# Kernel optimization log

Hardware: AMD Instinct MI355X
Metric: run time of the kernel (lower is better)

Reference implementation:

```python
import jax, jax.numpy as jnp
import numpy as np

ROPE_BASE = 10000.0

def _rope_tables(seq_len, head_dim, dtype):
    inv_freq = 1.0 / (ROPE_BASE ** (jnp.arange(0, head_dim, 2, dtype=jnp.float32) / head_dim))
    t = jnp.arange(seq_len, dtype=jnp.float32)
    freqs = jnp.einsum('s,d->sd', t, inv_freq)  # [S, D/2]
    return jnp.cos(freqs).astype(dtype), jnp.sin(freqs).astype(dtype)

def _apply_rope(x, cos, sin):
    # x: [B, H, S, D]; cos/sin: [S, D/2]
    half = x.shape[-1] // 2
    x1, x2 = x[..., :half], x[..., half:]
    c = cos[None, None, :, :]
    s = sin[None, None, :, :]
    return jnp.concatenate([x1 * c - x2 * s, x1 * s + x2 * c], axis=-1)

def setup_inputs() -> dict:
    key = jax.random.key(0)
    k1, k2, k3 = jax.random.split(key, 3)
    B, S, dim = 4, 2048, 1024
    x = jax.random.normal(k1, (B, S, dim), dtype=jnp.float32)
    Wqkv = jax.random.normal(k2, (3 * dim, dim), dtype=jnp.float32) * (1.0 / np.sqrt(dim))
    Wout = jax.random.normal(k3, (dim, dim), dtype=jnp.float32) * (1.0 / np.sqrt(dim))
    mask = jnp.tril(jnp.ones((S, S), dtype=bool))[None, None, :, :]  # causal [1,1,S,S]
    return {"x": x, "mask": mask, "Wqkv": Wqkv, "Wout": Wout, "n_heads": 16}

def reference(x, mask, Wqkv, Wout, n_heads):
    B, S, dim = x.shape
    H = n_heads
    D = dim // H
    qkv = jnp.einsum('bsd,ed->bse', x, Wqkv)             # [B,S,3*dim]
    qkv = qkv.reshape(B, S, 3, H, D)
    q = jnp.transpose(qkv[:, :, 0], (0, 2, 1, 3))        # [B,H,S,D]
    k = jnp.transpose(qkv[:, :, 1], (0, 2, 1, 3))
    v = jnp.transpose(qkv[:, :, 2], (0, 2, 1, 3))
    cos, sin = _rope_tables(S, D, x.dtype)
    q = _apply_rope(q, cos, sin)
    k = _apply_rope(k, cos, sin)
    scale = 1.0 / np.sqrt(D).astype(np.float32)
    scores = jnp.einsum('bhsd,bhtd->bhst', q, k) * scale  # [B,H,S,S]
    scores = jnp.where(mask, scores, -jnp.inf)
    attn = jax.nn.softmax(scores, axis=-1)
    out = jnp.einsum('bhst,bhtd->bhsd', attn, v)          # [B,H,S,D]
    out = jnp.transpose(out, (0, 2, 1, 3)).reshape(B, S, dim)
    return jnp.einsum('bsd,ed->bse', out, Wout)
```

## Files before the change

kernel.cpp:

```cpp
#include <hip/hip_runtime.h>
#include <math.h>


typedef __attribute__((ext_vector_type(8))) __bf16 bf16x8;
typedef __attribute__((ext_vector_type(8))) short  short8;
typedef __attribute__((ext_vector_type(4))) short  s16x4;
typedef __attribute__((ext_vector_type(4))) float  f32x4;

#define MFMA16(a, b, c) __builtin_amdgcn_mfma_f32_16x16x32_bf16((a), (b), (c), 0, 0, 0)

static constexpr int    BATCH = 4;
static constexpr int    SEQ   = 2048;
static constexpr int    DIM   = 1024;
static constexpr int    NH    = 16;
static constexpr int    HD    = 64;
static constexpr size_t BHSD  = (size_t)BATCH * NH * SEQ * HD;
static constexpr float  NEGINF = -1e9f;
static constexpr int    PS_LD  = 72;

__device__ __forceinline__ short f2bf(float f) {
    union { float f; unsigned u; } v; v.f = f;
    unsigned r = v.u + 0x7fffu + ((v.u >> 16) & 1u);
    return (short)(r >> 16);
}

__device__ __forceinline__ short8 cvt8(const f32x4 lo, const f32x4 hi) {
    short8 r;
    r[0] = f2bf(lo[0]); r[1] = f2bf(lo[1]); r[2] = f2bf(lo[2]); r[3] = f2bf(lo[3]);
    r[4] = f2bf(hi[0]); r[5] = f2bf(hi[1]); r[6] = f2bf(hi[2]); r[7] = f2bf(hi[3]);
    return r;
}

template <bool F32>
__device__ __forceinline__ short8 ld8(const void* p, size_t row, int K, int k) {
    if constexpr (F32) {
        const float* f = (const float*)p;
        f32x4 lo = *(const f32x4*)&f[row * (size_t)K + k];
        f32x4 hi = *(const f32x4*)&f[row * (size_t)K + k + 4];
        return cvt8(lo, hi);
    } else {
        const short* s = (const short*)p;
        return *(const short8*)&s[row * (size_t)K + k];
    }
}

__device__ __forceinline__ void gload16(const void* g, void* lds) {
    __builtin_amdgcn_global_load_lds(
        (const __attribute__((address_space(1))) void*)g,
        (__attribute__((address_space(3))) void*)lds, 16, 0, 0);
}

__global__ __launch_bounds__(256) void prep_kernel(
    const float* __restrict__ X, const float* __restrict__ Wq,
    const float* __restrict__ Wo, short* __restrict__ Xb,
    short* __restrict__ Wqb, short* __restrict__ Wob,
    float* __restrict__ cosT, float* __restrict__ sinT) {
    const int stride = gridDim.x * blockDim.x;
    for (int idx = blockIdx.x * blockDim.x + threadIdx.x; idx < 3211264; idx += stride) {
        if (idx < 3145728) {
            const float* src; short* dst; int off;
            if (idx < 2097152)      { src = X;  dst = Xb;  off = idx; }
            else if (idx < 2883584) { src = Wq; dst = Wqb; off = idx - 2097152; }
            else                    { src = Wo; dst = Wob; off = idx - 2883584; }
            f32x4 v = *(const f32x4*)&src[(size_t)off * 4];
            s16x4 r;
            r[0] = f2bf(v[0]); r[1] = f2bf(v[1]); r[2] = f2bf(v[2]); r[3] = f2bf(v[3]);
            *(s16x4*)&dst[(size_t)off * 4] = r;
        } else {
            int r = idx - 3145728;
            int s = r >> 5, d = r & 31;
            float ang = (float)s * __expf(-0.28782313662425574f * (float)d);
            float sn, cs;
            sincosf(ang, &sn, &cs);
            cosT[r] = cs; sinT[r] = sn;
        }
    }
}

template <bool AF32, bool BF32>
__device__ __forceinline__ void gemm128_core(
    const void* __restrict__ A, const void* __restrict__ B, int K,
    short* As, short* Bs, int bm, int bn, f32x4 acc[4][4]) {
    const int tid  = threadIdx.x;
    const int lane = tid & 63;
    const int wave = tid >> 6;
    const int quad = lane >> 4;
    const int col  = lane & 15;
    const int wm   = (wave & 1) * 64;
    const int wn   = (wave >> 1) * 64;

    const int r0 = tid >> 2;
    const int r1 = (tid + 256) >> 2;
    const int ko = (tid & 3) * 8;

#pragma unroll
    for (int i = 0; i < 4; ++i)
#pragma unroll
        for (int j = 0; j < 4; ++j) acc[i][j] = f32x4{0.f, 0.f, 0.f, 0.f};

#pragma unroll 1
    for (int k0 = 0; k0 < K; k0 += 32) {
        short8 a0 = ld8<AF32>(A, (size_t)(bm + r0), K, k0 + ko);
        short8 a1 = ld8<AF32>(A, (size_t)(bm + r1), K, k0 + ko);
        short8 b0 = ld8<BF32>(B, (size_t)(bn + r0), K, k0 + ko);
        short8 b1 = ld8<BF32>(B, (size_t)(bn + r1), K, k0 + ko);
        __syncthreads();
        *(short8*)&As[tid * 8]         = a0;
        *(short8*)&As[(tid + 256) * 8] = a1;
        *(short8*)&Bs[tid * 8]         = b0;
        *(short8*)&Bs[(tid + 256) * 8] = b1;
        __syncthreads();

        bf16x8 af[4], bfr[4];
#pragma unroll
        for (int i = 0; i < 4; ++i)
            af[i] = *(const bf16x8*)&As[(wm + i * 16 + col) * 32 + quad * 8];
#pragma unroll
        for (int j = 0; j < 4; ++j)
            bfr[j] = *(const bf16x8*)&Bs[(wn + j * 16 + col) * 32 + quad * 8];
#pragma unroll
        for (int i = 0; i < 4; ++i)
#pragma unroll
            for (int j = 0; j < 4; ++j)
                acc[i][j] = MFMA16(af[i], bfr[j], acc[i][j]);
    }
}

__device__ __forceinline__ void gemm128_p2(
    const short* __restrict__ A, const short* __restrict__ B, int K,
    short* As, short* Bs, int bm, int bn, f32x4 acc[4][4]) {
    const int tid  = threadIdx.x;
    const int lane = tid & 63;
    const int wave = tid >> 6;
    const int quad = lane >> 4;
    const int col  = lane & 15;
    const int wm   = (wave & 1) * 64;
    const int wn   = (wave >> 1) * 64;

    const int nt = K >> 6;
    const int rr = tid >> 3;
    const int swk = (((tid & 7) ^ (rr & 7)) << 3);
    const short* Ab = &A[(size_t)(bm + rr) * K + swk];
    const short* Bb = &B[(size_t)(bn + rr) * K + swk];

#pragma unroll
    for (int i = 0; i < 4; ++i)
#pragma unroll
        for (int j = 0; j < 4; ++j) acc[i][j] = f32x4{0.f, 0.f, 0.f, 0.f};

#define STAGE_TILE(c)                                                         \
    {                                                                         \
        const int s_ = (c) & 1;                                               \
        const int k0_ = (c) << 6;                                             \
        _Pragma("unroll")                                                     \
        for (int q = 0; q < 4; ++q) {                                         \
            gload16(Ab + (size_t)(q * 32) * K + k0_,                          \
                    &As[s_ * 8192 + q * 2048 + wave * 512]);                  \
            gload16(Bb + (size_t)(q * 32) * K + k0_,                          \
                    &Bs[s_ * 8192 + q * 2048 + wave * 512]);                  \
        }                                                                     \
    }

    STAGE_TILE(0);
    STAGE_TILE(1);

    const int pc0 = ((quad) ^ (col & 7)) << 3;
    const int pc1 = ((4 | quad) ^ (col & 7)) << 3;

#pragma unroll 1
    for (int c = 0; c < nt; ++c) {
        const int s = c & 1;
        if (c + 1 < nt) { asm volatile("s_waitcnt vmcnt(8)" ::: "memory"); }
        else            { asm volatile("s_waitcnt vmcnt(0)" ::: "memory"); }
        __builtin_amdgcn_s_barrier();

        const short* Asl = &As[s * 8192];
        const short* Bsl = &Bs[s * 8192];
        bf16x8 af[4][2], bfr[4][2];
#pragma unroll
        for (int i = 0; i < 4; ++i) {
            const int r = (wm + i * 16 + col) * 64;
            af[i][0] = *(const bf16x8*)&Asl[r + pc0];
            af[i][1] = *(const bf16x8*)&Asl[r + pc1];
        }
#pragma unroll
        for (int j = 0; j < 4; ++j) {
            const int r = (wn + j * 16 + col) * 64;
            bfr[j][0] = *(const bf16x8*)&Bsl[r + pc0];
            bfr[j][1] = *(const bf16x8*)&Bsl[r + pc1];
        }
#pragma unroll
        for (int kk = 0; kk < 2; ++kk)
#pragma unroll
            for (int i = 0; i < 4; ++i)
#pragma unroll
                for (int j = 0; j < 4; ++j)
                    acc[i][j] = MFMA16(af[i][kk], bfr[j][kk], acc[i][j]);

        __builtin_amdgcn_s_barrier();
        if (c + 2 < nt) STAGE_TILE(c + 2);
    }
#undef STAGE_TILE
}

template <bool PRE>
__global__ __launch_bounds__(256, 2) void qkv_rope_kernel(
    const void* __restrict__ X, const void* __restrict__ W,
    const float* __restrict__ cosT, const float* __restrict__ sinT,
    short* __restrict__ Qo, short* __restrict__ Ko, short* __restrict__ VT) {
    __shared__ __align__(16) short As[2 * 8192];
    __shared__ __align__(16) short Bs[2 * 8192];
    const int bm = blockIdx.y * 128, bn = blockIdx.x * 128;
    const int lane = threadIdx.x & 63, wave = threadIdx.x >> 6;
    const int quad = lane >> 4, col = lane & 15;
    const int wm = (wave & 1) * 64, wn = (wave >> 1) * 64;

    f32x4 acc[4][4];
    if constexpr (PRE)
        gemm128_p2((const short*)X, (const short*)W, 1024, As, Bs, bm, bn, acc);
    else
        gemm128_core<true, true>(X, W, 1024, As, Bs, bm, bn, acc);

    const int n0    = bn + wn;
    const int which = n0 >> 10;
    const int h     = (n0 >> 6) & 15;

    if (which == 2) {
#pragma unroll
        for (int i = 0; i < 4; ++i) {
            int    m = bm + wm + i * 16 + quad * 4;
            int    b = m >> 11, s = m & 2047;
            size_t rowb = (size_t)(b * NH + h) * HD;
#pragma unroll
            for (int j = 0; j < 4; ++j) {
                int   d = j * 16 + col;
                s16x4 pk;
                pk[0] = f2bf(acc[i][j][0]); pk[1] = f2bf(acc[i][j][1]);
                pk[2] = f2bf(acc[i][j][2]); pk[3] = f2bf(acc[i][j][3]);
                *(s16x4*)&VT[(rowb + d) * SEQ + s] = pk;
            }
        }
    } else {
        short* dst = which ? Ko : Qo;
#pragma unroll
        for (int i = 0; i < 4; ++i)
#pragma unroll
            for (int reg = 0; reg < 4; ++reg) {
                int    m = bm + wm + i * 16 + quad * 4 + reg;
                int    b = m >> 11, s = m & 2047;
                size_t base = ((size_t)(b * NH + h) * SEQ + s) * HD;
#pragma unroll
                for (int j = 0; j < 2; ++j) {
                    int   d1 = j * 16 + col;
                    float sn, cs;
                    if constexpr (PRE) {
                        cs = cosT[(s << 5) + d1];
                        sn = sinT[(s << 5) + d1];
                    } else {
                        float inv = __expf(-0.28782313662425574f * (float)d1);
                        sincosf((float)s * inv, &sn, &cs);
                    }
                    float x1 = acc[i][j][reg];
                    float x2 = acc[i][j + 2][reg];
                    dst[base + d1]      = f2bf(x1 * cs - x2 * sn);
                    dst[base + d1 + 32] = f2bf(x1 * sn + x2 * cs);
                }
            }
    }
}

__global__ __launch_bounds__(256, 2) void attn_kernel(
    const short* __restrict__ Q, const short* __restrict__ K,
    const short* __restrict__ VT, short* __restrict__ att) {
    const int b = blockIdx.z, h = blockIdx.y;
    const int tid = threadIdx.x, wave = tid >> 6, lane = tid & 63;
    const int quad = lane >> 4, col = lane & 15;
    const size_t hoff = (size_t)(b * NH + h) * SEQ * HD;
    const short* Qp  = Q + hoff;
    const short* Kp  = K + hoff;
    const short* VTp = VT + hoff;

    __shared__ __align__(16) short Kt[64 * 64];
    __shared__ __align__(16) short Vt[64 * 64];
    __shared__ __align__(16) short Ps[4 * 32 * PS_LD];

    const int r0 = tid >> 3;
    const int r1 = r0 + 32;
    const int c8 = (tid & 7) * 8;
    const int cs = c8 ^ ((r0 & 7) << 3);
    const int swc = (col & 7) << 3;
    const int cA  = (quad * 8) ^ swc;
    const int cB  = (32 + quad * 8) ^ swc;
    short* Pw = &Ps[wave * 32 * PS_LD];

#pragma unroll 1
    for (int pass = 0; pass < 2; ++pass) {
        const int qt   = pass ? 15 - (int)blockIdx.x : (int)blockIdx.x;
        const int q0   = qt * 128 + wave * 32;
        const int tmax = 2 * qt + 1;

        bf16x8 aq[2][2];
#pragma unroll
        for (int s2 = 0; s2 < 2; ++s2) {
            aq[s2][0] = *(const bf16x8*)&Qp[(q0 + s2 * 16 + col) * HD + quad * 8];
            aq[s2][1] = *(const bf16x8*)&Qp[(q0 + s2 * 16 + col) * HD + 32 + quad * 8];
        }

        float m_i[2][4], l_i[2][4];
        f32x4 o[2][4];
#pragma unroll
        for (int s2 = 0; s2 < 2; ++s2)
#pragma unroll
            for (int rr = 0; rr < 4; ++rr) {
                m_i[s2][rr] = NEGINF; l_i[s2][rr] = 0.f;
                o[s2][rr] = f32x4{0.f, 0.f, 0.f, 0.f};
            }

        short8 ka = *(const short8*)&Kp[r0 * HD + c8];
        short8 kb = *(const short8*)&Kp[r1 * HD + c8];
        short8 va = *(const short8*)&VTp[(size_t)r0 * SEQ + c8];
        short8 vb = *(const short8*)&VTp[(size_t)r1 * SEQ + c8];

#pragma unroll 1
        for (int t = 0; t <= tmax; ++t) {
            const int kt = t * 64;
            __syncthreads();
            *(short8*)&Kt[r0 * 64 + cs] = ka;
            *(short8*)&Kt[r1 * 64 + cs] = kb;
            *(short8*)&Vt[r0 * 64 + cs] = va;
            *(short8*)&Vt[r1 * 64 + cs] = vb;
            __syncthreads();

            if (t < tmax) {
                const int kn = kt + 64;
                ka = *(const short8*)&Kp[(kn + r0) * HD + c8];
                kb = *(const short8*)&Kp[(kn + r1) * HD + c8];
                va = *(const short8*)&VTp[(size_t)r0 * SEQ + kn + c8];
                vb = *(const short8*)&VTp[(size_t)r1 * SEQ + kn + c8];
            }

            if (kt > q0 + 31) continue;

            float p[2][4][4];
            __builtin_amdgcn_s_setprio(1);
#pragma unroll
            for (int jn = 0; jn < 4; ++jn) {
                bf16x8 b0 = *(const bf16x8*)&Kt[(jn * 16 + col) * 64 + cA];
                bf16x8 b1 = *(const bf16x8*)&Kt[(jn * 16 + col) * 64 + cB];
#pragma unroll
                for (int s2 = 0; s2 < 2; ++s2) {
                    f32x4 s = f32x4{0.f, 0.f, 0.f, 0.f};
                    s = MFMA16(aq[s2][0], b0, s);
                    s = MFMA16(aq[s2][1], b1, s);
                    if (t >= 2 * qt) {
#pragma unroll
                        for (int reg = 0; reg < 4; ++reg) {
                            int qr = q0 + s2 * 16 + quad * 4 + reg;
                            int kc = kt + jn * 16 + col;
                            p[s2][jn][reg] = (kc <= qr) ? s[reg] * 0.125f : NEGINF;
                        }
                    } else {
#pragma unroll
                        for (int reg = 0; reg < 4; ++reg)
                            p[s2][jn][reg] = s[reg] * 0.125f;
                    }
                }
            }
            __builtin_amdgcn_s_setprio(0);

#pragma unroll
            for (int s2 = 0; s2 < 2; ++s2) {
                float lm[4];
#pragma unroll
                for (int reg = 0; reg < 4; ++reg)
                    lm[reg] = fmaxf(fmaxf(p[s2][0][reg], p[s2][1][reg]),
                                    fmaxf(p[s2][2][reg], p[s2][3][reg]));
                int ok = (lm[0] <= m_i[s2][0] + 8.f) & (lm[1] <= m_i[s2][1] + 8.f) &
                         (lm[2] <= m_i[s2][2] + 8.f) & (lm[3] <= m_i[s2][3] + 8.f);
                if (__all(ok)) {
#pragma unroll
                    for (int reg = 0; reg < 4; ++reg) {
                        float rs = 0.f;
#pragma unroll
                        for (int jn = 0; jn < 4; ++jn) {
                            p[s2][jn][reg] = __expf(p[s2][jn][reg] - m_i[s2][reg]);
                            rs += p[s2][jn][reg];
                        }
                        l_i[s2][reg] += rs;
                    }
                } else {
                    float alpha[4];
#pragma unroll
                    for (int reg = 0; reg < 4; ++reg) {
                        float mx = lm[reg];
#pragma unroll
                        for (int off = 8; off >= 1; off >>= 1)
                            mx = fmaxf(mx, __shfl_xor(mx, off, 64));
                        float mn   = fmaxf(m_i[s2][reg], mx);
                        alpha[reg] = __expf(m_i[s2][reg] - mn);
                        float rs = 0.f;
#pragma unroll
                        for (int jn = 0; jn < 4; ++jn) {
                            p[s2][jn][reg] = __expf(p[s2][jn][reg] - mn);
                            rs += p[s2][jn][reg];
                        }
                        l_i[s2][reg] = l_i[s2][reg] * alpha[reg] + rs;
                        m_i[s2][reg] = mn;
                    }
#pragma unroll
                    for (int jd = 0; jd < 4; ++jd)
#pragma unroll
                        for (int reg = 0; reg < 4; ++reg)
                            o[s2][jd][reg] *= alpha[reg];
                }

#pragma unroll
                for (int jn = 0; jn < 4; ++jn)
#pragma unroll
                    for (int reg = 0; reg < 4; ++reg)
                        Pw[(s2 * 16 + quad * 4 + reg) * PS_LD + jn * 16 + col] =
                            f2bf(p[s2][jn][reg]);
            }

            bf16x8 ap[2][2];
#pragma unroll
            for (int s2 = 0; s2 < 2; ++s2) {
                ap[s2][0] = *(const bf16x8*)&Pw[(s2 * 16 + col) * PS_LD + quad * 8];
                ap[s2][1] = *(const bf16x8*)&Pw[(s2 * 16 + col) * PS_LD + 32 + quad * 8];
            }
            __builtin_amdgcn_s_setprio(1);
#pragma unroll
            for (int jd = 0; jd < 4; ++jd) {
                bf16x8 bv0 = *(const bf16x8*)&Vt[(jd * 16 + col) * 64 + cA];
                bf16x8 bv1 = *(const bf16x8*)&Vt[(jd * 16 + col) * 64 + cB];
#pragma unroll
                for (int s2 = 0; s2 < 2; ++s2) {
                    o[s2][jd] = MFMA16(ap[s2][0], bv0, o[s2][jd]);
                    o[s2][jd] = MFMA16(ap[s2][1], bv1, o[s2][jd]);
                }
            }
            __builtin_amdgcn_s_setprio(0);
        }

#pragma unroll
        for (int s2 = 0; s2 < 2; ++s2) {
#pragma unroll
            for (int off = 8; off >= 1; off >>= 1)
#pragma unroll
                for (int reg = 0; reg < 4; ++reg)
                    l_i[s2][reg] += __shfl_xor(l_i[s2][reg], off, 64);
            float inv_l[4];
#pragma unroll
            for (int reg = 0; reg < 4; ++reg) inv_l[reg] = 1.f / l_i[s2][reg];
#pragma unroll
            for (int jd = 0; jd < 4; ++jd)
#pragma unroll
                for (int reg = 0; reg < 4; ++reg) {
                    int s = q0 + s2 * 16 + quad * 4 + reg;
                    att[((size_t)(b * SEQ + s)) * DIM + h * HD + jd * 16 + col] =
                        f2bf(o[s2][jd][reg] * inv_l[reg]);
                }
        }
    }
}

template <bool PRE>
__global__ __launch_bounds__(256, 2) void out_gemm_kernel(
    const short* __restrict__ A, const void* __restrict__ W,
    float* __restrict__ out) {
    __shared__ __align__(16) short As[2 * 8192];
    __shared__ __align__(16) short Bs[2 * 8192];
    const int bm = blockIdx.y * 128, bn = blockIdx.x * 128;
    const int lane = threadIdx.x & 63, wave = threadIdx.x >> 6;
    const int quad = lane >> 4, col = lane & 15;
    const int wm = (wave & 1) * 64, wn = (wave >> 1) * 64;

    f32x4 acc[4][4];
    if constexpr (PRE)
        gemm128_p2(A, (const short*)W, 1024, As, Bs, bm, bn, acc);
    else
        gemm128_core<false, true>(A, W, 1024, As, Bs, bm, bn, acc);

#pragma unroll
    for (int i = 0; i < 4; ++i)
#pragma unroll
        for (int reg = 0; reg < 4; ++reg) {
            int    m    = bm + wm + i * 16 + quad * 4 + reg;
            size_t base = (size_t)m * DIM + bn + wn;
#pragma unroll
            for (int j = 0; j < 4; ++j)
                out[base + j * 16 + col] = acc[i][j][reg];
        }
}

extern "C" void kernel_launch(void* const* d_in, const int* in_sizes, int n_in,
                              void* d_out, int out_size, void* d_ws, size_t ws_size,
                              hipStream_t stream) {
    const float* x    = nullptr;
    const float* Wqkv = nullptr;
    const float* Wout = nullptr;
    for (int i = 0; i < n_in; ++i) {
        switch (in_sizes[i]) {
            case 8388608: x    = (const float*)d_in[i]; break;
            case 3145728: Wqkv = (const float*)d_in[i]; break;
            case 1048576: Wout = (const float*)d_in[i]; break;
            default: break;
        }
    }
    if (!x || !Wqkv || !Wout) return;

    short* Q  = (short*)d_ws;
    short* K  = Q + BHSD;
    short* VT = K + BHSD;
    float* out = (float*)d_out;

    const size_t need_pre = (size_t)4 * BHSD * sizeof(short)
                          + BHSD * sizeof(short)
                          + (size_t)3145728 * sizeof(short)
                          + (size_t)1048576 * sizeof(short)
                          + (size_t)2 * 65536 * sizeof(float);

    if (ws_size >= need_pre) {
        short* att  = VT + BHSD;
        short* Xb   = att + BHSD;
        short* Wqb  = Xb + BHSD;
        short* Wob  = Wqb + 3145728;
        float* cosT = (float*)(Wob + 1048576);
        float* sinT = cosT + 65536;

        prep_kernel<<<dim3(2048), 256, 0, stream>>>(x, Wqkv, Wout, Xb, Wqb, Wob, cosT, sinT);
        qkv_rope_kernel<true><<<dim3(24, 64), 256, 0, stream>>>(Xb, Wqb, cosT, sinT, Q, K, VT);
        attn_kernel<<<dim3(8, NH, BATCH), 256, 0, stream>>>(Q, K, VT, att);
        out_gemm_kernel<true><<<dim3(8, 64), 256, 0, stream>>>(att, Wob, out);
    } else {
        qkv_rope_kernel<false><<<dim3(24, 64), 256, 0, stream>>>(
            x, Wqkv, nullptr, nullptr, Q, K, VT);

        const bool direct = ws_size >= (size_t)4 * BHSD * sizeof(short);
        short* att_dst = direct ? (VT + BHSD) : (short*)d_out;
        attn_kernel<<<dim3(8, NH, BATCH), 256, 0, stream>>>(Q, K, VT, att_dst);

        short* att = att_dst;
        if (!direct) {
            att = (short*)d_ws;
            hipMemcpyAsync(att, att_dst, BHSD * sizeof(short), hipMemcpyDeviceToDevice, stream);
        }
        out_gemm_kernel<false><<<dim3(8, 64), 256, 0, stream>>>(att, Wout, out);
    }
}
```

Baseline: 278.1 us.

## Add 256x256-tile 8-wave QKV+RoPE GEMM with phased prefetch pipeline

Adds a new QKV projection kernel that uses 256x256 output tiles, 512 threads and 128 KB of dynamic LDS. Global-to-LDS staging is interleaved across eight sub-phases per iteration with explicit vmcnt waits, and s_setprio is raised around the MFMA blocks. The larger tile raises operand reuse and cuts the grid from 1536 to 384 blocks. In exchange it needs the big dynamic-LDS attribute, which limits occupancy to one block per CU and may leave some of the 256 CUs idle with only 384 blocks.

Result: no change. 281.2 us (+1.1%).

```diff
diff --git a/kernel.cpp b/kernel.cpp
--- a/kernel.cpp
+++ b/kernel.cpp
@@ -203,6 +203,158 @@
 #undef STAGE_TILE
 }
 
+__global__ __launch_bounds__(512, 2) void qkv_rope_256(
+    const short* __restrict__ X, const short* __restrict__ W,
+    const float* __restrict__ cosT, const float* __restrict__ sinT,
+    short* __restrict__ Qo, short* __restrict__ Ko, short* __restrict__ VT) {
+    extern __shared__ __align__(16) short smem[];
+    short* As = smem;
+    short* Bs = smem + 32768;
+
+    const int tid  = threadIdx.x;
+    const int lane = tid & 63;
+    const int wave = tid >> 6;
+    const int quad = lane >> 4;
+    const int col  = lane & 15;
+    const int wmh  = wave >> 2;
+    const int wn4  = wave & 3;
+    const int bhalf = wn4 >> 1;
+    const int rbb   = (wn4 & 1) * 64;
+
+    const int bm = blockIdx.y * 256;
+    const int bn = blockIdx.x * 256;
+
+    const int srow = tid >> 3;
+    const int ssw  = (((tid & 7) ^ (srow & 7)) << 3);
+    const short* Arow = &X[(size_t)(bm + srow) * 1024 + ssw];
+    const short* Brow = &W[(size_t)(bn + srow) * 1024 + ssw];
+    const int ldst = (wave * 8) * 64;
+
+#define STG_A(t, hf, buf)                                                     \
+    { _Pragma("unroll") for (int g = 0; g < 2; ++g)                           \
+        gload16(Arow + (size_t)((hf) * 128 + g * 64) * 1024 + (t) * 64,       \
+                &As[(buf) * 16384 + (hf) * 8192 + g * 4096 + ldst]); }
+#define STG_B(t, hf, buf)                                                     \
+    { _Pragma("unroll") for (int g = 0; g < 2; ++g)                           \
+        gload16(Brow + (size_t)((hf) * 128 + g * 64) * 1024 + (t) * 64,       \
+                &Bs[(buf) * 16384 + (hf) * 8192 + g * 4096 + ldst]); }
+
+    f32x4 acc[8][4];
+#pragma unroll
+    for (int i = 0; i < 8; ++i)
+#pragma unroll
+        for (int j = 0; j < 4; ++j) acc[i][j] = f32x4{0.f, 0.f, 0.f, 0.f};
+
+    const int pck0 = ((quad) ^ (col & 7)) << 3;
+    const int pck1 = ((4 | quad) ^ (col & 7)) << 3;
+
+    STG_A(0, 0, 0); STG_A(0, 1, 0); STG_B(0, 0, 0); STG_B(0, 1, 0);
+    STG_B(1, 0, 1); STG_B(1, 1, 1); STG_A(1, 0, 1);
+    asm volatile("s_waitcnt vmcnt(6)" ::: "memory");
+    __builtin_amdgcn_s_barrier();
+
+    bf16x8 bfr[4][2];
+
+#pragma unroll 1
+    for (int it = 0; it < 8; ++it) {
+        const bool last = (it == 7);
+        const int t0 = 2 * it;
+#pragma unroll
+        for (int bh = 0; bh < 2; ++bh) {
+            const int buf = bh;
+#pragma unroll
+            for (int q = 0; q < 4; ++q) {
+                const int ph = bh * 4 + q + 1;
+                if (q == 0) {
+#pragma unroll
+                    for (int nj = 0; nj < 4; ++nj) {
+                        const int r = (rbb + nj * 16 + col) * 64;
+                        bfr[nj][0] = *(const bf16x8*)&Bs[buf * 16384 + bhalf * 8192 + r + pck0];
+                        bfr[nj][1] = *(const bf16x8*)&Bs[buf * 16384 + bhalf * 8192 + r + pck1];
+                    }
+                }
+                bf16x8 af[2][2];
+#pragma unroll
+                for (int m2 = 0; m2 < 2; ++m2) {
+                    const int r = ((q * 2 + m2) * 16 + col) * 64;
+                    af[m2][0] = *(const bf16x8*)&As[buf * 16384 + wmh * 8192 + r + pck0];
+                    af[m2][1] = *(const bf16x8*)&As[buf * 16384 + wmh * 8192 + r + pck1];
+                }
+                if (ph == 1) { STG_A(t0 + 1, 1, 1); }
+                else if (ph == 2) { if (!last) STG_B(t0 + 2, 0, 0); }
+                else if (ph == 3) { if (!last) STG_B(t0 + 2, 1, 0); }
+                else if (ph == 4) {
+                    if (!last) { STG_A(t0 + 2, 0, 0);
+                                 asm volatile("s_waitcnt vmcnt(6)" ::: "memory"); }
+                    else       { asm volatile("s_waitcnt vmcnt(0)" ::: "memory"); }
+                }
+                else if (ph == 5) { if (!last) STG_A(t0 + 2, 1, 0); }
+                else if (ph == 6) { if (!last) STG_B(t0 + 3, 0, 1); }
+                else if (ph == 7) { if (!last) STG_B(t0 + 3, 1, 1); }
+                else {
+                    if (!last) { STG_A(t0 + 3, 0, 1);
+                                 asm volatile("s_waitcnt vmcnt(6)" ::: "memory"); }
+                }
+                __builtin_amdgcn_s_barrier();
+                __builtin_amdgcn_s_setprio(1);
+#pragma unroll
+                for (int kk = 0; kk < 2; ++kk)
+#pragma unroll
+                    for (int m2 = 0; m2 < 2; ++m2)
+#pragma unroll
+                        for (int nj = 0; nj < 4; ++nj)
+                            acc[q * 2 + m2][nj] =
+                                MFMA16(af[m2][kk], bfr[nj][kk], acc[q * 2 + m2][nj]);
+                __builtin_amdgcn_s_setprio(0);
+                __builtin_amdgcn_s_barrier();
+            }
+        }
+    }
+#undef STG_A
+#undef STG_B
+
+    const int n0    = bn + wn4 * 64;
+    const int which = n0 >> 10;
+    const int h     = (n0 >> 6) & 15;
+
+    if (which == 2) {
+#pragma unroll
+        for (int mi = 0; mi < 8; ++mi) {
+            int    m = bm + wmh * 128 + mi * 16 + quad * 4;
+            int    b = m >> 11, s = m & 2047;
+            size_t rowb = (size_t)(b * NH + h) * HD;
+#pragma unroll
+            for (int j = 0; j < 4; ++j) {
+                int   d = j * 16 + col;
+                s16x4 pk;
+                pk[0] = f2bf(acc[mi][j][0]); pk[1] = f2bf(acc[mi][j][1]);
+                pk[2] = f2bf(acc[mi][j][2]); pk[3] = f2bf(acc[mi][j][3]);
+                *(s16x4*)&VT[(rowb + d) * SEQ + s] = pk;
+            }
+        }
+    } else {
+        short* dst = which ? Ko : Qo;
+#pragma unroll
+        for (int mi = 0; mi < 8; ++mi)
+#pragma unroll
+            for (int reg = 0; reg < 4; ++reg) {
+                int    m = bm + wmh * 128 + mi * 16 + quad * 4 + reg;
+                int    b = m >> 11, s = m & 2047;
+                size_t base = ((size_t)(b * NH + h) * SEQ + s) * HD;
+#pragma unroll
+                for (int j = 0; j < 2; ++j) {
+                    int   d1 = j * 16 + col;
+                    float cs = cosT[(s << 5) + d1];
+                    float sn = sinT[(s << 5) + d1];
+                    float x1 = acc[mi][j][reg];
+                    float x2 = acc[mi][j + 2][reg];
+                    dst[base + d1]      = f2bf(x1 * cs - x2 * sn);
+                    dst[base + d1 + 32] = f2bf(x1 * sn + x2 * cs);
+                }
+            }
+    }
+}
+
 template <bool PRE>
 __global__ __launch_bounds__(256, 2) void qkv_rope_kernel(
     const void* __restrict__ X, const void* __restrict__ W,
@@ -520,6 +672,13 @@
                           + (size_t)1048576 * sizeof(short)
                           + (size_t)2 * 65536 * sizeof(float);
 
+    static int big_lds = -1;
+    if (big_lds < 0) {
+        big_lds = (hipFuncSetAttribute((const void*)qkv_rope_256,
+                       hipFuncAttributeMaxDynamicSharedMemorySize,
+                       131072) == hipSuccess) ? 1 : 0;
+    }
+
     if (ws_size >= need_pre) {
         short* att  = VT + BHSD;
         short* Xb   = att + BHSD;
@@ -529,7 +688,12 @@
         float* sinT = cosT + 65536;
 
         prep_kernel<<<dim3(2048), 256, 0, stream>>>(x, Wqkv, Wout, Xb, Wqb, Wob, cosT, sinT);
-        qkv_rope_kernel<true><<<dim3(24, 64), 256, 0, stream>>>(Xb, Wqb, cosT, sinT, Q, K, VT);
+        if (big_lds)
+            qkv_rope_256<<<dim3(12, 32), 512, 131072, stream>>>(
+                Xb, Wqb, cosT, sinT, Q, K, VT);
+        else
+            qkv_rope_kernel<true><<<dim3(24, 64), 256, 0, stream>>>(
+                Xb, Wqb, cosT, sinT, Q, K, VT);
         attn_kernel<<<dim3(8, NH, BATCH), 256, 0, stream>>>(Q, K, VT, att);
         out_gemm_kernel<true><<<dim3(8, 64), 256, 0, stream>>>(att, Wob, out);
     } else {
```
